# Kernel tuning notes

Measured on AMD Instinct MI355X. Metric: run time of the kernel, lower is better.

The kernel has to match this reference:

```python
import jax, jax.numpy as jnp
import numpy as np

B, NINP, NMAX, C = 32, 16, 128, 128

def conv1x1(x, w, b):
    # x: [B, cin, n, n], w: [cout, cin], b: [cout]
    return jnp.einsum('bchw,oc->bohw', x, w) + b[None, :, None, None]

def block(x, Msum, wa, ba, wb, bb, wc, bc):
    x1 = jax.nn.relu(conv1x1(x, wa, ba) * Msum)
    x2 = jax.nn.relu(conv1x1(x, wb, bb) * Msum)
    x1x2 = jnp.matmul(x1, x2) * Msum          # batched [B,C,n,n] @ [B,C,n,n]
    return jax.nn.relu(conv1x1(jnp.concatenate([x1x2, x], axis=1), wc, bc) * Msum)

def setup_inputs() -> dict:
    key = jax.random.key(0)
    ks = jax.random.split(key, 32)
    def w(k, o, i, s=0.05):
        return jax.random.normal(k, (o, i), dtype=jnp.float32) * s
    inp = {
        'X2': jax.random.normal(ks[0], (B, NINP, NMAX, NMAX), dtype=jnp.float32),
        'M':  jax.random.uniform(ks[1], (B, 2, NMAX, NMAX), dtype=jnp.float32),
        'w11': w(ks[2], C, NINP), 'b11': jnp.zeros((C,), jnp.float32),
        'w12': w(ks[3], C, NINP), 'b12': jnp.zeros((C,), jnp.float32),
        'w13': w(ks[4], C, C + NINP), 'b13': jnp.zeros((C,), jnp.float32),
        'w21': w(ks[5], C, C), 'b21': jnp.zeros((C,), jnp.float32),
        'w22': w(ks[6], C, C), 'b22': jnp.zeros((C,), jnp.float32),
        'w23': w(ks[7], C, 2 * C), 'b23': jnp.zeros((C,), jnp.float32),
        'w31': w(ks[8], C, C), 'b31': jnp.zeros((C,), jnp.float32),
        'w32': w(ks[9], C, C), 'b32': jnp.zeros((C,), jnp.float32),
        'w33': w(ks[10], C, 2 * C), 'b33': jnp.zeros((C,), jnp.float32),
        'h1w': w(ks[11], 32, 3 * C), 'h1b': jnp.zeros((32,), jnp.float32),
        'h2w': w(ks[12], 1, 32), 'h2b': jnp.zeros((1,), jnp.float32),
    }
    return inp

def reference(X2, M, w11, b11, w12, b12, w13, b13, w21, b21, w22, b22, w23, b23,
              w31, b31, w32, b32, w33, b33, h1w, h1b, h2w, h2b):
    Msum = jnp.sum(M, axis=1, keepdims=True)   # [B,1,n,n]
    Mdiag = M[:, 0:1]                          # [B,1,n,n]
    x = X2
    x = block(x, Msum, w11, b11, w12, b12, w13, b13)
    xo1 = jnp.sum(x * Mdiag, axis=(2, 3))      # [B,C]
    x = block(x, Msum, w21, b21, w22, b22, w23, b23)
    xo2 = jnp.sum(x * Mdiag, axis=(2, 3))
    x = block(x, Msum, w31, b31, w32, b32, w33, b33)
    xo3 = jnp.sum(x * Mdiag, axis=(2, 3))
    h = jnp.concatenate([xo1, xo2, xo3], axis=1)
    h = jax.nn.relu(h @ h1w.T + h1b)
    return h @ h2w.T + h2b                     # [B,1]
```

## Files before the change

### kernel.cpp

```cpp
#include <hip/hip_runtime.h>
#include <stdint.h>
#include <stddef.h>

#define NBATCH 32
#define HW     16384
#define CCH    128
#define WROW   40
#define WCHUNK 10240

typedef short bf16x8 __attribute__((ext_vector_type(8)));
typedef float f32x4  __attribute__((ext_vector_type(4)));

__device__ __forceinline__ float bf2f(unsigned short u){
    union { unsigned int i; float f; } v; v.i = ((unsigned int)u) << 16; return v.f;
}
__device__ __forceinline__ unsigned short f2bf(float f){
    union { float f; unsigned int i; } v; v.f = f;
    unsigned int x = v.i;
    x += 0x7fffu + ((x >> 16) & 1u);
    return (unsigned short)(x >> 16);
}
__device__ __forceinline__ unsigned int h16(uint2 u, int j){
    unsigned int v = (j & 2) ? u.y : u.x;
    return (j & 1) ? (v >> 16) : (v & 0xffffu);
}
__device__ __forceinline__ void gl_lds16(const unsigned short* g, unsigned short* l){
    __builtin_amdgcn_global_load_lds(
        reinterpret_cast<const __attribute__((address_space(1))) unsigned int*>(
            reinterpret_cast<uintptr_t>(g)),
        reinterpret_cast<__attribute__((address_space(3))) unsigned int*>(
            reinterpret_cast<uintptr_t>(l)),
        16, 0, 0);
}

#define WPREP_TOTAL 399360
__global__ __launch_bounds__(256) void k_prep(
    const float* __restrict__ w11, const float* __restrict__ w12, const float* __restrict__ w13,
    const float* __restrict__ w21, const float* __restrict__ w22, const float* __restrict__ w23,
    const float* __restrict__ w31, const float* __restrict__ w32, const float* __restrict__ w33,
    unsigned short* __restrict__ wp)
{
    int i = blockIdx.x*256 + threadIdx.x;
    if(i >= WPREP_TOTAL) return;
    const float* src; int K, mode, base;
    if     (i < 10240) { src=w11; K=16;  mode=1; base=0;      }
    else if(i < 20480) { src=w12; K=16;  mode=1; base=10240;  }
    else if(i < 71680) { src=w13; K=144; mode=2; base=20480;  }
    else if(i < 112640){ src=w21; K=128; mode=0; base=71680;  }
    else if(i < 153600){ src=w22; K=128; mode=0; base=112640; }
    else if(i < 235520){ src=w23; K=256; mode=0; base=153600; }
    else if(i < 276480){ src=w31; K=128; mode=0; base=235520; }
    else if(i < 317440){ src=w32; K=128; mode=0; base=276480; }
    else               { src=w33; K=256; mode=0; base=317440; }
    int j  = i - base;
    int ck = j / WCHUNK;
    int jj = j - ck*WCHUNK;
    int half = jj / 5120;
    int rr   = (jj / WROW) & 127;
    int c    = jj % WROW;
    float v = 0.f;
    if(c < 32){
        int col = (mode==1) ? (c & 15)
                : (mode==2) ? (ck < 4 ? ck*32 + c : 128 + (c & 15))
                :             ck*32 + c;
        v = src[rr*K + col];
    }
    unsigned short hi = f2bf(v);
    wp[i] = half ? f2bf(v - bf2f(hi)) : hi;
}

__global__ __launch_bounds__(256) void k_msum(const float* __restrict__ M, float* __restrict__ msum){
    int i = blockIdx.x*256 + threadIdx.x;
    int b = i >> 14, hw = i & (HW-1);
    msum[i] = M[(size_t)b*2*HW + hw] + M[(size_t)b*2*HW + HW + hw];
}

template<int NCHP, int NCHX, bool CC, bool XS>
__global__ __launch_bounds__(256,2) void k_conv(
    const unsigned short* __restrict__ Wp,
    const unsigned short* __restrict__ Psrc,
    const void* __restrict__ Xsrc,
    const float* __restrict__ biasA, const float* __restrict__ biasB,
    const float* __restrict__ msum, const float* __restrict__ Mfull,
    unsigned short* __restrict__ OutA, unsigned short* __restrict__ OutB,
    float* __restrict__ xo, int b0, int xo_off)
{
    constexpr int NCH = NCHP + NCHX;
    __shared__ unsigned short Wl[2*WCHUNK];
    __shared__ unsigned short Xt[256*WROW];
    const int bi = blockIdx.y, bg = b0 + bi;
    const int hw0 = blockIdx.x * 256;
    const int z = CC ? 0 : blockIdx.z;
    const int t = threadIdx.x;
    const int w = t >> 6, l = t & 63;
    const int lr = l & 15, lg = l >> 4;
    const int wm = w & 1, wn = w >> 1;
    const int cg = t & 3, h4 = t >> 2;
    const unsigned short* Wseg  = Wp + (size_t)z*NCH*WCHUNK;
    const unsigned short* pbase = (NCHP > 0) ? (Psrc + (size_t)bi*CCH*HW) : nullptr;
    const float* xfbase = nullptr;
    const unsigned short* xbbase = nullptr;
    if constexpr (XS) xfbase = (const float*)Xsrc + (size_t)bg*16*HW;
    else              xbbase = (const unsigned short*)Xsrc + (size_t)bi*CCH*HW;

    f32x4 acc[4][8];
    #pragma unroll
    for(int mf=0; mf<4; mf++)
        #pragma unroll
        for(int nf=0; nf<8; nf++) acc[mf][nf] = (f32x4){0.f,0.f,0.f,0.f};

    uint2 xr0[8], xr1[8];
    float xf0[16], xf1[16];

    auto wdma = [&](int ck){
        const unsigned short* src = Wseg + (size_t)ck*WCHUNK + (size_t)t*8;
        unsigned short* dstl = &Wl[(ck & 1)*WCHUNK + t*8];
        #pragma unroll
        for(int r=0; r<5; r++)
            gl_lds16(src + (size_t)r*2048, dstl + r*2048);
    };
    auto loadXb = [&](int ck, uint2 (&xr)[8]){
        const unsigned short* s = ((ck < NCHP) ? (pbase + (size_t)ck*32*HW)
                                               : (xbbase + (size_t)(ck-NCHP)*32*HW))
                                  + hw0 + h4*4;
        #pragma unroll
        for(int i=0;i<8;i++) xr[i] = *reinterpret_cast<const uint2*>(s + (size_t)(cg*8+i)*HW);
    };
    auto loadXf = [&](float (&xf)[16]){
        const float* s = xfbase + hw0 + t;
        #pragma unroll
        for(int c=0;c<16;c++) xf[c] = s[(size_t)c*HW];
    };
    auto writeXb = [&](uint2 (&xr)[8]){
        #pragma unroll
        for(int j=0;j<4;j++){
            uint4 pk;
            pk.x = h16(xr[0],j) | (h16(xr[1],j) << 16);
            pk.y = h16(xr[2],j) | (h16(xr[3],j) << 16);
            pk.z = h16(xr[4],j) | (h16(xr[5],j) << 16);
            pk.w = h16(xr[6],j) | (h16(xr[7],j) << 16);
            *reinterpret_cast<uint4*>(&Xt[(h4*4+j)*WROW + cg*8]) = pk;
        }
    };
    auto writeXf = [&](float (&xf)[16]){
        unsigned int hi[16], lo[16];
        #pragma unroll
        for(int c=0;c<16;c++){
            unsigned short h = f2bf(xf[c]);
            hi[c] = h;
            lo[c] = f2bf(xf[c] - bf2f(h));
        }
        uint4 a, b2, c4, d;
        a.x  = hi[0] |(hi[1] <<16); a.y  = hi[2] |(hi[3] <<16); a.z  = hi[4] |(hi[5] <<16); a.w  = hi[6] |(hi[7] <<16);
        b2.x = hi[8] |(hi[9] <<16); b2.y = hi[10]|(hi[11]<<16); b2.z = hi[12]|(hi[13]<<16); b2.w = hi[14]|(hi[15]<<16);
        c4.x = lo[0] |(lo[1] <<16); c4.y = lo[2] |(lo[3] <<16); c4.z = lo[4] |(lo[5] <<16); c4.w = lo[6] |(lo[7] <<16);
        d.x  = lo[8] |(lo[9] <<16); d.y  = lo[10]|(lo[11]<<16); d.z  = lo[12]|(lo[13]<<16); d.w  = lo[14]|(lo[15]<<16);
        unsigned short* base = &Xt[t*WROW];
        *reinterpret_cast<uint4*>(base +  0) = a;
        *reinterpret_cast<uint4*>(base +  8) = b2;
        *reinterpret_cast<uint4*>(base + 16) = c4;
        *reinterpret_cast<uint4*>(base + 24) = d;
    };
    auto do_load = [&](int ck, uint2 (&xr)[8], float (&xf)[16]){
        if(ck < NCHP) loadXb(ck, xr);
        else if constexpr (XS) loadXf(xf);
        else loadXb(ck, xr);
    };
    auto do_write = [&](int ck, uint2 (&xr)[8], float (&xf)[16]){
        if(ck < NCHP) writeXb(xr);
        else if constexpr (XS) writeXf(xf);
        else writeXb(xr);
    };
    auto compute = [&](int ck){
        const unsigned short* Wb = &Wl[(ck & 1)*WCHUNK];
        bf16x8 ah[4], al[4];
        #pragma unroll
        for(int mf=0; mf<4; mf++){
            ah[mf] = *reinterpret_cast<const bf16x8*>(&Wb[(wm*64 + mf*16 + lr)*WROW + lg*8]);
            al[mf] = *reinterpret_cast<const bf16x8*>(&Wb[(128 + wm*64 + mf*16 + lr)*WROW + lg*8]);
        }
        #pragma unroll
        for(int nf=0; nf<8; nf++){
            bf16x8 bfr = *reinterpret_cast<const bf16x8*>(&Xt[(wn*128 + nf*16 + lr)*WROW + lg*8]);
            #pragma unroll
            for(int mf=0; mf<4; mf++){
                acc[mf][nf] = __builtin_amdgcn_mfma_f32_16x16x32_bf16(ah[mf], bfr, acc[mf][nf], 0,0,0);
                acc[mf][nf] = __builtin_amdgcn_mfma_f32_16x16x32_bf16(al[mf], bfr, acc[mf][nf], 0,0,0);
            }
        }
    };

    wdma(0);
    do_load(0, xr0, xf0);

    #pragma unroll
    for(int ck=0; ck<NCH; ck+=2){
        do_write(ck, xr0, xf0);
        asm volatile("s_waitcnt vmcnt(0) lgkmcnt(0)" ::: "memory");
        __builtin_amdgcn_s_barrier();
        if(ck+1 < NCH){ wdma(ck+1); do_load(ck+1, xr1, xf1); }
        compute(ck);
        __builtin_amdgcn_s_barrier();
        if(ck+1 < NCH){
            do_write(ck+1, xr1, xf1);
            asm volatile("s_waitcnt vmcnt(0) lgkmcnt(0)" ::: "memory");
            __builtin_amdgcn_s_barrier();
            if(ck+2 < NCH){ wdma(ck+2); do_load(ck+2, xr0, xf0); }
            compute(ck+1);
            __builtin_amdgcn_s_barrier();
        }
    }

    float msv[8], mdv[8];
    #pragma unroll
    for(int nf=0; nf<8; nf++){
        int hwi = hw0 + wn*128 + nf*16 + lr;
        msv[nf] = msum[(size_t)bg*HW + hwi];
        if constexpr (CC) mdv[nf] = Mfull[(size_t)bg*2*HW + hwi];
    }
    const float* bias = z ? biasB : biasA;
    unsigned short* dst = (z ? OutB : OutA) + (size_t)bi*CCH*HW;
    #pragma unroll
    for(int mf=0; mf<4; mf++){
        float red[4] = {0.f,0.f,0.f,0.f};
        #pragma unroll
        for(int reg=0; reg<4; reg++){
            int row = wm*64 + mf*16 + lg*4 + reg;
            float bv = bias[row];
            #pragma unroll
            for(int nf=0; nf<8; nf++){
                float v2 = (acc[mf][nf][reg] + bv) * msv[nf];
                v2 = v2 > 0.f ? v2 : 0.f;
                dst[(size_t)row*HW + hw0 + wn*128 + nf*16 + lr] = f2bf(v2);
                if constexpr (CC) red[reg] += v2 * mdv[nf];
            }
        }
        if constexpr (CC){
            #pragma unroll
            for(int reg=0; reg<4; reg++){
                float r = red[reg];
                r += __shfl_xor(r, 1);
                r += __shfl_xor(r, 2);
                r += __shfl_xor(r, 4);
                r += __shfl_xor(r, 8);
                if(lr == 0)
                    atomicAdd(&xo[(size_t)bg*384 + xo_off + wm*64 + mf*16 + lg*4 + reg], r);
            }
        }
    }
}

__global__ __launch_bounds__(256) void k_bmm(
    const unsigned short* __restrict__ A, const unsigned short* __restrict__ Bm,
    const float* __restrict__ msum, unsigned short* __restrict__ P, int b0)
{
    __shared__ unsigned short Bs[128*136];
    const int m  = blockIdx.x;
    const int bi = m >> 7;
    const int bg = b0 + bi;
    const unsigned short* Ab = A  + (size_t)m*HW;
    const unsigned short* Bb = Bm + (size_t)m*HW;
    unsigned short*       Pb = P  + (size_t)m*HW;
    const float* ms = msum + (size_t)bg*HW;
    const int t = threadIdx.x;
    const int w  = t >> 6;
    const int l  = t & 63;
    const int lr = l & 15;
    const int lg = l >> 4;

    bf16x8 af[4][2];
    #pragma unroll
    for(int kk=0;kk<4;kk++)
        #pragma unroll
        for(int rt=0;rt<2;rt++)
            af[kk][rt] = *reinterpret_cast<const bf16x8*>(Ab + (size_t)(w*32 + rt*16 + lr)*128 + kk*32 + lg*8);

    #pragma unroll
    for(int it=0; it<8; it++){
        int task = it*256 + t;
        int j  = task & 127;
        int kg = task >> 7;
        unsigned short v[8];
        #pragma unroll
        for(int i=0;i<8;i++) v[i] = Bb[(size_t)(kg*8+i)*128 + j];
        uint4 pk;
        pk.x = (unsigned int)v[0] | ((unsigned int)v[1]<<16);
        pk.y = (unsigned int)v[2] | ((unsigned int)v[3]<<16);
        pk.z = (unsigned int)v[4] | ((unsigned int)v[5]<<16);
        pk.w = (unsigned int)v[6] | ((unsigned int)v[7]<<16);
        *reinterpret_cast<uint4*>(&Bs[j*136 + kg*8]) = pk;
    }
    __syncthreads();

    f32x4 acc[2][8];
    #pragma unroll
    for(int rt=0;rt<2;rt++)
        #pragma unroll
        for(int ct=0;ct<8;ct++) acc[rt][ct] = (f32x4){0.f,0.f,0.f,0.f};

    #pragma unroll
    for(int kk=0;kk<4;kk++){
        #pragma unroll
        for(int ct=0;ct<8;ct++){
            bf16x8 bfr = *reinterpret_cast<const bf16x8*>(&Bs[(ct*16+lr)*136 + kk*32 + lg*8]);
            acc[0][ct] = __builtin_amdgcn_mfma_f32_16x16x32_bf16(af[kk][0], bfr, acc[0][ct], 0,0,0);
            acc[1][ct] = __builtin_amdgcn_mfma_f32_16x16x32_bf16(af[kk][1], bfr, acc[1][ct], 0,0,0);
        }
    }
    #pragma unroll
    for(int rt=0;rt<2;rt++){
        #pragma unroll
        for(int ct=0;ct<8;ct++){
            #pragma unroll
            for(int r=0;r<4;r++){
                int row = w*32 + rt*16 + lg*4 + r;
                int col = ct*16 + lr;
                float v = acc[rt][ct][r] * ms[row*128 + col];
                Pb[(size_t)row*128 + col] = f2bf(v);
            }
        }
    }
}

__global__ __launch_bounds__(1024) void k_head(
    const float* __restrict__ xo, const float* __restrict__ h1w, const float* __restrict__ h1b,
    const float* __restrict__ h2w, const float* __restrict__ h2b, float* __restrict__ out)
{
    __shared__ float hbuf[NBATCH][32];
    const int t = threadIdx.x;
    const int b = t >> 5, j = t & 31;
    float a = h1b[j];
    #pragma unroll 8
    for(int k=0;k<384;k++) a += xo[b*384+k]*h1w[j*384+k];
    a = a > 0.f ? a : 0.f;
    hbuf[b][j] = a;
    __syncthreads();
    if(j == 0){
        float s = h2b[0];
        #pragma unroll
        for(int k=0;k<32;k++) s += hbuf[b][k]*h2w[k];
        out[b] = s;
    }
}

extern "C" void kernel_launch(void* const* d_in, const int* in_sizes, int n_in,
                              void* d_out, int out_size, void* d_ws, size_t ws_size,
                              hipStream_t stream)
{
    (void)in_sizes; (void)n_in; (void)out_size;
    const float* X2  = (const float*)d_in[0];
    const float* M   = (const float*)d_in[1];
    const float* w11 = (const float*)d_in[2];  const float* b11 = (const float*)d_in[3];
    const float* w12 = (const float*)d_in[4];  const float* b12 = (const float*)d_in[5];
    const float* w13 = (const float*)d_in[6];  const float* b13 = (const float*)d_in[7];
    const float* w21 = (const float*)d_in[8];  const float* b21 = (const float*)d_in[9];
    const float* w22 = (const float*)d_in[10]; const float* b22 = (const float*)d_in[11];
    const float* w23 = (const float*)d_in[12]; const float* b23 = (const float*)d_in[13];
    const float* w31 = (const float*)d_in[14]; const float* b31 = (const float*)d_in[15];
    const float* w32 = (const float*)d_in[16]; const float* b32 = (const float*)d_in[17];
    const float* w33 = (const float*)d_in[18]; const float* b33 = (const float*)d_in[19];
    const float* h1w = (const float*)d_in[20]; const float* h1b = (const float*)d_in[21];
    const float* h2w = (const float*)d_in[22]; const float* h2b = (const float*)d_in[23];
    float* out = (float*)d_out;

    char* ws = (char*)d_ws;
    size_t off = 0;
    float* msum = (float*)(ws + off); off += (size_t)NBATCH*HW*4;
    float* xo   = (float*)(ws + off); off += (size_t)NBATCH*384*4;
    unsigned short* wp = (unsigned short*)(ws + off); off += (size_t)WPREP_TOTAL*2;
    off = (off + 255) & ~(size_t)255;

    int bc = 32;
    while (bc > 1 && off + 3ull*(size_t)bc*CCH*HW*2 > ws_size) bc >>= 1;
    size_t bufb = (size_t)bc*CCH*HW*2;
    unsigned short* buf0 = (unsigned short*)(ws + off);
    unsigned short* buf1 = (unsigned short*)(ws + off + bufb);
    unsigned short* buf2 = (unsigned short*)(ws + off + 2*bufb);

    const unsigned short* Wa1 = wp + 0;
    const unsigned short* Wc1 = wp + 20480;
    const unsigned short* Wa2 = wp + 71680;
    const unsigned short* Wc2 = wp + 153600;
    const unsigned short* Wa3 = wp + 235520;
    const unsigned short* Wc3 = wp + 317440;

    k_prep<<<(WPREP_TOTAL+255)/256, 256, 0, stream>>>(w11,w12,w13,w21,w22,w23,w31,w32,w33, wp);
    k_msum<<<(NBATCH*HW)/256, 256, 0, stream>>>(M, msum);
    hipMemsetAsync(xo, 0, (size_t)NBATCH*384*4, stream);

    for(int b0 = 0; b0 < NBATCH; b0 += bc){
        dim3 gab(HW/256, bc, 2);
        dim3 gcc(HW/256, bc);
        dim3 gmat(bc*CCH);
        k_conv<0,1,false,true ><<<gab, 256, 0, stream>>>(Wa1, nullptr, X2, b11, b12, msum, M, buf0, buf1, nullptr, b0, 0);
        k_bmm<<<gmat, 256, 0, stream>>>(buf0, buf1, msum, buf0, b0);
        k_conv<4,1,true ,true ><<<gcc, 256, 0, stream>>>(Wc1, buf0, X2, b13, b13, msum, M, buf1, nullptr, xo, b0, 0);
        k_conv<0,4,false,false><<<gab, 256, 0, stream>>>(Wa2, nullptr, buf1, b21, b22, msum, M, buf2, buf0, nullptr, b0, 0);
        k_bmm<<<gmat, 256, 0, stream>>>(buf2, buf0, msum, buf2, b0);
        k_conv<4,4,true ,false><<<gcc, 256, 0, stream>>>(Wc2, buf2, buf1, b23, b23, msum, M, buf0, nullptr, xo, b0, 128);
        k_conv<0,4,false,false><<<gab, 256, 0, stream>>>(Wa3, nullptr, buf0, b31, b32, msum, M, buf1, buf2, nullptr, b0, 0);
        k_bmm<<<gmat, 256, 0, stream>>>(buf1, buf2, msum, buf1, b0);
        k_conv<4,4,true ,false><<<gcc, 256, 0, stream>>>(Wc3, buf1, buf0, b33, b33, msum, M, buf2, nullptr, xo, b0, 256);
    }
    k_head<<<1, 1024, 0, stream>>>(xo, h1w, h1b, h2w, h2b, out);
}
```

Measured before the change: 1.174 ms.

## Pre-swizzle conv inputs into LDS-ready tiles and retile conv to 512 threads

Conv outputs that feed the next block and the input X2 are now written in a pre-tiled, XOR-swizzled bf16 hi/lo layout. The next conv can DMA them straight into LDS with global_load_lds instead of loading registers and transposing. Weight packing drops row padding in favour of the same XOR swizzle to avoid bank conflicts. The conv kernel moves to 512 threads with a smaller per-wave tile and a finer vmcnt-based pipeline. In exchange it adds an X2 prep kernel, an extra workspace buffer and more complex swizzle indexing, and the last block skips storing its output.

```diff
diff --git a/kernel.cpp b/kernel.cpp
--- a/kernel.cpp
+++ b/kernel.cpp
@@ -5,8 +5,6 @@
 #define NBATCH 32
 #define HW     16384
 #define CCH    128
-#define WROW   40
-#define WCHUNK 10240
 
 typedef short bf16x8 __attribute__((ext_vector_type(8)));
 typedef float f32x4  __attribute__((ext_vector_type(4)));
@@ -32,8 +30,11 @@
             reinterpret_cast<uintptr_t>(l)),
         16, 0, 0);
 }
-
-#define WPREP_TOTAL 399360
+template<int N> __device__ __forceinline__ void vmwait(){
+    asm volatile("s_waitcnt vmcnt(%0)" :: "n"(N) : "memory");
+}
+
+#define WPREP_TOTAL 319488
 __global__ __launch_bounds__(256) void k_prep(
     const float* __restrict__ w11, const float* __restrict__ w12, const float* __restrict__ w13,
     const float* __restrict__ w21, const float* __restrict__ w22, const float* __restrict__ w23,
@@ -43,30 +44,53 @@
     int i = blockIdx.x*256 + threadIdx.x;
     if(i >= WPREP_TOTAL) return;
     const float* src; int K, mode, base;
-    if     (i < 10240) { src=w11; K=16;  mode=1; base=0;      }
-    else if(i < 20480) { src=w12; K=16;  mode=1; base=10240;  }
-    else if(i < 71680) { src=w13; K=144; mode=2; base=20480;  }
-    else if(i < 112640){ src=w21; K=128; mode=0; base=71680;  }
-    else if(i < 153600){ src=w22; K=128; mode=0; base=112640; }
-    else if(i < 235520){ src=w23; K=256; mode=0; base=153600; }
-    else if(i < 276480){ src=w31; K=128; mode=0; base=235520; }
-    else if(i < 317440){ src=w32; K=128; mode=0; base=276480; }
-    else               { src=w33; K=256; mode=0; base=317440; }
+    if     (i < 8192)  { src=w11; K=16;  mode=1; base=0;      }
+    else if(i < 16384) { src=w12; K=16;  mode=1; base=8192;   }
+    else if(i < 57344) { src=w13; K=144; mode=2; base=16384;  }
+    else if(i < 90112) { src=w21; K=128; mode=0; base=57344;  }
+    else if(i < 122880){ src=w22; K=128; mode=0; base=90112;  }
+    else if(i < 188416){ src=w23; K=256; mode=0; base=122880; }
+    else if(i < 221184){ src=w31; K=128; mode=0; base=188416; }
+    else if(i < 253952){ src=w32; K=128; mode=0; base=221184; }
+    else               { src=w33; K=256; mode=0; base=253952; }
     int j  = i - base;
-    int ck = j / WCHUNK;
-    int jj = j - ck*WCHUNK;
-    int half = jj / 5120;
-    int rr   = (jj / WROW) & 127;
-    int c    = jj % WROW;
-    float v = 0.f;
-    if(c < 32){
-        int col = (mode==1) ? (c & 15)
-                : (mode==2) ? (ck < 4 ? ck*32 + c : 128 + (c & 15))
-                :             ck*32 + c;
-        v = src[rr*K + col];
-    }
+    int ck = j >> 13;
+    int jj = j & 8191;
+    int half = jj >> 12;
+    int row  = (jj >> 5) & 127;
+    int cs   = jj & 31;
+    int s    = (row >> 1) & 3;
+    int c    = (((cs >> 3) ^ s) << 3) | (cs & 7);
+    int col  = (mode==1) ? (c & 15)
+             : (mode==2) ? (ck < 4 ? ck*32 + c : 128 + (c & 15))
+             :             ck*32 + c;
+    float v = src[row*K + col];
     unsigned short hi = f2bf(v);
     wp[i] = half ? f2bf(v - bf2f(hi)) : hi;
+}
+
+__global__ __launch_bounds__(256) void k_xprep(const float* __restrict__ X2, unsigned short* __restrict__ X2b){
+    const int ht = blockIdx.x, b = blockIdx.y, t = threadIdx.x;
+    const float* src = X2 + (size_t)b*16*HW + ht*256 + t;
+    unsigned short hv[16], lv[16];
+    #pragma unroll
+    for(int c=0;c<16;c++){
+        float v = src[(size_t)c*HW];
+        hv[c] = f2bf(v);
+        lv[c] = f2bf(v - bf2f(hv[c]));
+    }
+    const int s = (t >> 1) & 3;
+    unsigned short* dst = X2b + ((size_t)b*64 + ht)*8192 + t*32;
+    #pragma unroll
+    for(int g=0; g<4; g++){
+        const unsigned short* q = (g < 2) ? &hv[(g&1)*8] : &lv[(g&1)*8];
+        uint4 pk;
+        pk.x = (unsigned int)q[0] | ((unsigned int)q[1]<<16);
+        pk.y = (unsigned int)q[2] | ((unsigned int)q[3]<<16);
+        pk.z = (unsigned int)q[4] | ((unsigned int)q[5]<<16);
+        pk.w = (unsigned int)q[6] | ((unsigned int)q[7]<<16);
+        *reinterpret_cast<uint4*>(dst + ((g ^ s) << 3)) = pk;
+    }
 }
 
 __global__ __launch_bounds__(256) void k_msum(const float* __restrict__ M, float* __restrict__ msum){
@@ -75,167 +99,155 @@
     msum[i] = M[(size_t)b*2*HW + hw] + M[(size_t)b*2*HW + HW + hw];
 }
 
-template<int NCHP, int NCHX, bool CC, bool XS>
-__global__ __launch_bounds__(256,2) void k_conv(
+template<int NCHP, int NCHX, bool CC, bool GX, bool STORE>
+__global__ __launch_bounds__(512,4) void k_conv(
     const unsigned short* __restrict__ Wp,
     const unsigned short* __restrict__ Psrc,
-    const void* __restrict__ Xsrc,
+    const unsigned short* __restrict__ Xsrc,
     const float* __restrict__ biasA, const float* __restrict__ biasB,
     const float* __restrict__ msum, const float* __restrict__ Mfull,
     unsigned short* __restrict__ OutA, unsigned short* __restrict__ OutB,
     float* __restrict__ xo, int b0, int xo_off)
 {
     constexpr int NCH = NCHP + NCHX;
-    __shared__ unsigned short Wl[2*WCHUNK];
-    __shared__ unsigned short Xt[256*WROW];
-    const int bi = blockIdx.y, bg = b0 + bi;
-    const int hw0 = blockIdx.x * 256;
+    __shared__ unsigned short Wl[16384];
+    __shared__ unsigned short Xl[16384];
+    const int bi = blockIdx.y, bg = b0 + bi, ht = blockIdx.x;
     const int z = CC ? 0 : blockIdx.z;
     const int t = threadIdx.x;
-    const int w = t >> 6, l = t & 63;
-    const int lr = l & 15, lg = l >> 4;
+    const int w = t >> 6, lane = t & 63;
+    const int lr = lane & 15, lg = lane >> 4;
     const int wm = w & 1, wn = w >> 1;
-    const int cg = t & 3, h4 = t >> 2;
-    const unsigned short* Wseg  = Wp + (size_t)z*NCH*WCHUNK;
-    const unsigned short* pbase = (NCHP > 0) ? (Psrc + (size_t)bi*CCH*HW) : nullptr;
-    const float* xfbase = nullptr;
-    const unsigned short* xbbase = nullptr;
-    if constexpr (XS) xfbase = (const float*)Xsrc + (size_t)bg*16*HW;
-    else              xbbase = (const unsigned short*)Xsrc + (size_t)bi*CCH*HW;
-
-    f32x4 acc[4][8];
+    const int cg = t & 7, h4 = t >> 3;
+    const unsigned short* Wseg  = Wp + (size_t)z*NCH*8192;
+    const unsigned short* pbase = Psrc + (size_t)bi*CCH*HW;
+    const unsigned short* xbase = Xsrc + ((size_t)(GX ? bg : bi)*64 + ht)*NCHX*8192;
+
+    f32x4 acc[4][4];
     #pragma unroll
     for(int mf=0; mf<4; mf++)
         #pragma unroll
-        for(int nf=0; nf<8; nf++) acc[mf][nf] = (f32x4){0.f,0.f,0.f,0.f};
-
-    uint2 xr0[8], xr1[8];
-    float xf0[16], xf1[16];
-
-    auto wdma = [&](int ck){
-        const unsigned short* src = Wseg + (size_t)ck*WCHUNK + (size_t)t*8;
-        unsigned short* dstl = &Wl[(ck & 1)*WCHUNK + t*8];
-        #pragma unroll
-        for(int r=0; r<5; r++)
-            gl_lds16(src + (size_t)r*2048, dstl + r*2048);
+        for(int nf=0; nf<4; nf++) acc[mf][nf] = (f32x4){0.f,0.f,0.f,0.f};
+
+    uint2 pr[2][4];
+
+    auto stage = [&](int ck){
+        { const unsigned short* s = Wseg + (size_t)ck*8192 + t*8;
+          unsigned short* d = &Wl[(ck&1)*8192] + t*8;
+          gl_lds16(s, d); gl_lds16(s + 4096, d + 4096); }
+        if(ck < NCHP){
+            const unsigned short* s = pbase + (size_t)(ck*32 + cg*4)*HW + ht*256 + h4*4;
+            #pragma unroll
+            for(int i2=0;i2<4;i2++) pr[ck&1][i2] = *reinterpret_cast<const uint2*>(s + (size_t)i2*HW);
+        } else {
+            const unsigned short* s = xbase + (size_t)(ck - NCHP)*8192 + t*8;
+            unsigned short* d = &Xl[(ck&1)*8192] + t*8;
+            gl_lds16(s, d); gl_lds16(s + 4096, d + 4096);
+        }
     };
-    auto loadXb = [&](int ck, uint2 (&xr)[8]){
-        const unsigned short* s = ((ck < NCHP) ? (pbase + (size_t)ck*32*HW)
-                                               : (xbbase + (size_t)(ck-NCHP)*32*HW))
-                                  + hw0 + h4*4;
-        #pragma unroll
-        for(int i=0;i<8;i++) xr[i] = *reinterpret_cast<const uint2*>(s + (size_t)(cg*8+i)*HW);
+    auto writeP = [&](int ck){
+        #pragma unroll
+        for(int j=0;j<4;j++){
+            int hwin = h4*4 + j;
+            int sx = (hwin >> 1) & 3;
+            int pos = (((cg>>1) ^ sx) << 3) + (cg&1)*4;
+            uint2 v;
+            v.x = h16(pr[ck&1][0],j) | (h16(pr[ck&1][1],j) << 16);
+            v.y = h16(pr[ck&1][2],j) | (h16(pr[ck&1][3],j) << 16);
+            *reinterpret_cast<uint2*>(&Xl[(ck&1)*8192] + hwin*32 + pos) = v;
+        }
     };
-    auto loadXf = [&](float (&xf)[16]){
-        const float* s = xfbase + hw0 + t;
-        #pragma unroll
-        for(int c=0;c<16;c++) xf[c] = s[(size_t)c*HW];
+    auto compute = [&](int buf){
+        const unsigned short* Wb = &Wl[buf*8192];
+        const unsigned short* Xb = &Xl[buf*8192];
+        #pragma unroll
+        for(int hp=0; hp<2; hp++){
+            bf16x8 ah[2], al[2];
+            #pragma unroll
+            for(int m2=0;m2<2;m2++){
+                int row = wm*64 + (hp*2+m2)*16 + lr;
+                int off = row*32 + ((lg ^ ((row>>1)&3)) << 3);
+                ah[m2] = *reinterpret_cast<const bf16x8*>(&Wb[off]);
+                al[m2] = *reinterpret_cast<const bf16x8*>(&Wb[4096 + off]);
+            }
+            #pragma unroll
+            for(int nf=0;nf<4;nf++){
+                int hwin = wn*64 + nf*16 + lr;
+                bf16x8 bfr = *reinterpret_cast<const bf16x8*>(&Xb[hwin*32 + ((lg ^ ((hwin>>1)&3)) << 3)]);
+                #pragma unroll
+                for(int m2=0;m2<2;m2++){
+                    acc[hp*2+m2][nf] = __builtin_amdgcn_mfma_f32_16x16x32_bf16(ah[m2], bfr, acc[hp*2+m2][nf], 0,0,0);
+                    acc[hp*2+m2][nf] = __builtin_amdgcn_mfma_f32_16x16x32_bf16(al[m2], bfr, acc[hp*2+m2][nf], 0,0,0);
+                }
+            }
+        }
     };
-    auto writeXb = [&](uint2 (&xr)[8]){
-        #pragma unroll
-        for(int j=0;j<4;j++){
-            uint4 pk;
-            pk.x = h16(xr[0],j) | (h16(xr[1],j) << 16);
-            pk.y = h16(xr[2],j) | (h16(xr[3],j) << 16);
-            pk.z = h16(xr[4],j) | (h16(xr[5],j) << 16);
-            pk.w = h16(xr[6],j) | (h16(xr[7],j) << 16);
-            *reinterpret_cast<uint4*>(&Xt[(h4*4+j)*WROW + cg*8]) = pk;
-        }
-    };
-    auto writeXf = [&](float (&xf)[16]){
-        unsigned int hi[16], lo[16];
-        #pragma unroll
-        for(int c=0;c<16;c++){
-            unsigned short h = f2bf(xf[c]);
-            hi[c] = h;
-            lo[c] = f2bf(xf[c] - bf2f(h));
-        }
-        uint4 a, b2, c4, d;
-        a.x  = hi[0] |(hi[1] <<16); a.y  = hi[2] |(hi[3] <<16); a.z  = hi[4] |(hi[5] <<16); a.w  = hi[6] |(hi[7] <<16);
-        b2.x = hi[8] |(hi[9] <<16); b2.y = hi[10]|(hi[11]<<16); b2.z = hi[12]|(hi[13]<<16); b2.w = hi[14]|(hi[15]<<16);
-        c4.x = lo[0] |(lo[1] <<16); c4.y = lo[2] |(lo[3] <<16); c4.z = lo[4] |(lo[5] <<16); c4.w = lo[6] |(lo[7] <<16);
-        d.x  = lo[8] |(lo[9] <<16); d.y  = lo[10]|(lo[11]<<16); d.z  = lo[12]|(lo[13]<<16); d.w  = lo[14]|(lo[15]<<16);
-        unsigned short* base = &Xt[t*WROW];
-        *reinterpret_cast<uint4*>(base +  0) = a;
-        *reinterpret_cast<uint4*>(base +  8) = b2;
-        *reinterpret_cast<uint4*>(base + 16) = c4;
-        *reinterpret_cast<uint4*>(base + 24) = d;
-    };
-    auto do_load = [&](int ck, uint2 (&xr)[8], float (&xf)[16]){
-        if(ck < NCHP) loadXb(ck, xr);
-        else if constexpr (XS) loadXf(xf);
-        else loadXb(ck, xr);
-    };
-    auto do_write = [&](int ck, uint2 (&xr)[8], float (&xf)[16]){
-        if(ck < NCHP) writeXb(xr);
-        else if constexpr (XS) writeXf(xf);
-        else writeXb(xr);
-    };
-    auto compute = [&](int ck){
-        const unsigned short* Wb = &Wl[(ck & 1)*WCHUNK];
-        bf16x8 ah[4], al[4];
-        #pragma unroll
-        for(int mf=0; mf<4; mf++){
-            ah[mf] = *reinterpret_cast<const bf16x8*>(&Wb[(wm*64 + mf*16 + lr)*WROW + lg*8]);
-            al[mf] = *reinterpret_cast<const bf16x8*>(&Wb[(128 + wm*64 + mf*16 + lr)*WROW + lg*8]);
-        }
-        #pragma unroll
-        for(int nf=0; nf<8; nf++){
-            bf16x8 bfr = *reinterpret_cast<const bf16x8*>(&Xt[(wn*128 + nf*16 + lr)*WROW + lg*8]);
-            #pragma unroll
-            for(int mf=0; mf<4; mf++){
-                acc[mf][nf] = __builtin_amdgcn_mfma_f32_16x16x32_bf16(ah[mf], bfr, acc[mf][nf], 0,0,0);
-                acc[mf][nf] = __builtin_amdgcn_mfma_f32_16x16x32_bf16(al[mf], bfr, acc[mf][nf], 0,0,0);
-            }
-        }
-    };
-
-    wdma(0);
-    do_load(0, xr0, xf0);
-
-    #pragma unroll
-    for(int ck=0; ck<NCH; ck+=2){
-        do_write(ck, xr0, xf0);
-        asm volatile("s_waitcnt vmcnt(0) lgkmcnt(0)" ::: "memory");
+
+    stage(0);
+    #pragma unroll
+    for(int i=0;i<NCH;i++){
+        if(i+1 < NCH) stage(i+1);
+        if(i+1 < NCH){ if(i+1 < NCHP) vmwait<6>(); else vmwait<4>(); }
+        else vmwait<0>();
+        __builtin_amdgcn_sched_barrier(0);
+        if(i < NCHP) writeP(i);
+        asm volatile("s_waitcnt lgkmcnt(0)" ::: "memory");
         __builtin_amdgcn_s_barrier();
-        if(ck+1 < NCH){ wdma(ck+1); do_load(ck+1, xr1, xf1); }
-        compute(ck);
+        compute(i & 1);
         __builtin_amdgcn_s_barrier();
-        if(ck+1 < NCH){
-            do_write(ck+1, xr1, xf1);
-            asm volatile("s_waitcnt vmcnt(0) lgkmcnt(0)" ::: "memory");
-            __builtin_amdgcn_s_barrier();
-            if(ck+2 < NCH){ wdma(ck+2); do_load(ck+2, xr0, xf0); }
-            compute(ck+1);
-            __builtin_amdgcn_s_barrier();
-        }
-    }
-
-    float msv[8], mdv[8];
-    #pragma unroll
-    for(int nf=0; nf<8; nf++){
-        int hwi = hw0 + wn*128 + nf*16 + lr;
+    }
+
+    float msv[4], mdv[4];
+    #pragma unroll
+    for(int nf=0; nf<4; nf++){
+        int hwi = ht*256 + wn*64 + nf*16 + lr;
         msv[nf] = msum[(size_t)bg*HW + hwi];
         if constexpr (CC) mdv[nf] = Mfull[(size_t)bg*2*HW + hwi];
     }
-    const float* bias = z ? biasB : biasA;
-    unsigned short* dst = (z ? OutB : OutA) + (size_t)bi*CCH*HW;
-    #pragma unroll
-    for(int mf=0; mf<4; mf++){
-        float red[4] = {0.f,0.f,0.f,0.f};
-        #pragma unroll
-        for(int reg=0; reg<4; reg++){
-            int row = wm*64 + mf*16 + lg*4 + reg;
-            float bv = bias[row];
-            #pragma unroll
-            for(int nf=0; nf<8; nf++){
-                float v2 = (acc[mf][nf][reg] + bv) * msv[nf];
-                v2 = v2 > 0.f ? v2 : 0.f;
-                dst[(size_t)row*HW + hw0 + wn*128 + nf*16 + lr] = f2bf(v2);
-                if constexpr (CC) red[reg] += v2 * mdv[nf];
-            }
-        }
-        if constexpr (CC){
+    if constexpr (!CC){
+        const float* bias = z ? biasB : biasA;
+        unsigned short* dst = (z ? OutB : OutA) + (size_t)bi*CCH*HW;
+        #pragma unroll
+        for(int mf=0; mf<4; mf++){
+            #pragma unroll
+            for(int reg=0; reg<4; reg++){
+                int row = wm*64 + mf*16 + lg*4 + reg;
+                float bv = bias[row];
+                #pragma unroll
+                for(int nf=0; nf<4; nf++){
+                    float v2 = (acc[mf][nf][reg] + bv) * msv[nf];
+                    v2 = v2 > 0.f ? v2 : 0.f;
+                    dst[(size_t)row*HW + ht*256 + wn*64 + nf*16 + lr] = f2bf(v2);
+                }
+            }
+        }
+    } else {
+        #pragma unroll
+        for(int mf=0; mf<4; mf++){
+            const int ckO = wm*2 + (mf>>1);
+            const int c0  = (mf&1)*16 + lg*4;
+            float red[4] = {0.f,0.f,0.f,0.f};
+            #pragma unroll
+            for(int nf=0; nf<4; nf++){
+                int hwin = wn*64 + nf*16 + lr;
+                float vv[4];
+                #pragma unroll
+                for(int reg=0; reg<4; reg++){
+                    int row = wm*64 + mf*16 + lg*4 + reg;
+                    float v2 = (acc[mf][nf][reg] + biasA[row]) * msv[nf];
+                    v2 = v2 > 0.f ? v2 : 0.f;
+                    vv[reg] = v2;
+                    red[reg] += v2 * mdv[nf];
+                }
+                if constexpr (STORE){
+                    int sx = (hwin>>1)&3;
+                    int pos = ((((c0>>3) ^ sx) << 3)) + (c0 & 7);
+                    uint2 pk;
+                    pk.x = (unsigned int)f2bf(vv[0]) | ((unsigned int)f2bf(vv[1])<<16);
+                    pk.y = (unsigned int)f2bf(vv[2]) | ((unsigned int)f2bf(vv[3])<<16);
+                    *reinterpret_cast<uint2*>(OutA + (((size_t)bi*64 + ht)*4 + ckO)*8192 + hwin*32 + pos) = pk;
+                }
+            }
             #pragma unroll
             for(int reg=0; reg<4; reg++){
                 float r = red[reg];
@@ -367,40 +379,44 @@
     size_t off = 0;
     float* msum = (float*)(ws + off); off += (size_t)NBATCH*HW*4;
     float* xo   = (float*)(ws + off); off += (size_t)NBATCH*384*4;
-    unsigned short* wp = (unsigned short*)(ws + off); off += (size_t)WPREP_TOTAL*2;
+    unsigned short* wp  = (unsigned short*)(ws + off); off += (size_t)WPREP_TOTAL*2;
     off = (off + 255) & ~(size_t)255;
+    unsigned short* X2b = (unsigned short*)(ws + off); off += (size_t)NBATCH*64*8192*2;
+    off = (off + 255) & ~(size_t)255;
 
     int bc = 32;
-    while (bc > 1 && off + 3ull*(size_t)bc*CCH*HW*2 > ws_size) bc >>= 1;
+    while (bc > 1 && off + 4ull*(size_t)bc*CCH*HW*2 > ws_size) bc >>= 1;
     size_t bufb = (size_t)bc*CCH*HW*2;
-    unsigned short* buf0 = (unsigned short*)(ws + off);
-    unsigned short* buf1 = (unsigned short*)(ws + off + bufb);
-    unsigned short* buf2 = (unsigned short*)(ws + off + 2*bufb);
-
-    const unsigned short* Wa1 = wp + 0;
-    const unsigned short* Wc1 = wp + 20480;
-    const unsigned short* Wa2 = wp + 71680;
-    const unsigned short* Wc2 = wp + 153600;
-    const unsigned short* Wa3 = wp + 235520;
-    const unsigned short* Wc3 = wp + 317440;
+    unsigned short* bufA = (unsigned short*)(ws + off);
+    unsigned short* bufB = (unsigned short*)(ws + off + bufb);
+    unsigned short* Xs1  = (unsigned short*)(ws + off + 2*bufb);
+    unsigned short* Xs2  = (unsigned short*)(ws + off + 3*bufb);
+
+    const unsigned short* Wab1 = wp + 0;
+    const unsigned short* Wc1  = wp + 16384;
+    const unsigned short* Wab2 = wp + 57344;
+    const unsigned short* Wc2  = wp + 122880;
+    const unsigned short* Wab3 = wp + 188416;
+    const unsigned short* Wc3  = wp + 253952;
 
     k_prep<<<(WPREP_TOTAL+255)/256, 256, 0, stream>>>(w11,w12,w13,w21,w22,w23,w31,w32,w33, wp);
+    k_xprep<<<dim3(64, NBATCH), 256, 0, stream>>>(X2, X2b);
     k_msum<<<(NBATCH*HW)/256, 256, 0, stream>>>(M, msum);
     hipMemsetAsync(xo, 0, (size_t)NBATCH*384*4, stream);
 
     for(int b0 = 0; b0 < NBATCH; b0 += bc){
-        dim3 gab(HW/256, bc, 2);
-        dim3 gcc(HW/256, bc);
+        dim3 gab(64, bc, 2);
+        dim3 gcc(64, bc, 1);
         dim3 gmat(bc*CCH);
-        k_conv<0,1,false,true ><<<gab, 256, 0, stream>>>(Wa1, nullptr, X2, b11, b12, msum, M, buf0, buf1, nullptr, b0, 0);
-        k_bmm<<<gmat, 256, 0, stream>>>(buf0, buf1, msum, buf0, b0);
-        k_conv<4,1,true ,true ><<<gcc, 256, 0, stream>>>(Wc1, buf0, X2, b13, b13, msum, M, buf1, nullptr, xo, b0, 0);
-        k_conv<0,4,false,false><<<gab, 256, 0, stream>>>(Wa2, nullptr, buf1, b21, b22, msum, M, buf2, buf0, nullptr, b0, 0);
-        k_bmm<<<gmat, 256, 0, stream>>>(buf2, buf0, msum, buf2, b0);
-        k_conv<4,4,true ,false><<<gcc, 256, 0, stream>>>(Wc2, buf2, buf1, b23, b23, msum, M, buf0, nullptr, xo, b0, 128);
-        k_conv<0,4,false,false><<<gab, 256, 0, stream>>>(Wa3, nullptr, buf0, b31, b32, msum, M, buf1, buf2, nullptr, b0, 0);
-        k_bmm<<<gmat, 256, 0, stream>>>(buf1, buf2, msum, buf1, b0);
-        k_conv<4,4,true ,false><<<gcc, 256, 0, stream>>>(Wc3, buf1, buf0, b33, b33, msum, M, buf2, nullptr, xo, b0, 256);
+        k_conv<0,1,false,true ,true ><<<gab, 512, 0, stream>>>(Wab1, bufA, X2b, b11, b12, msum, M, bufA, bufB, xo, b0, 0);
+        k_bmm<<<gmat, 256, 0, stream>>>(bufA, bufB, msum, bufA, b0);
+        k_conv<4,1,true ,true ,true ><<<gcc, 512, 0, stream>>>(Wc1, bufA, X2b, b13, b13, msum, M, Xs1, nullptr, xo, b0, 0);
+        k_conv<0,4,false,false,true ><<<gab, 512, 0, stream>>>(Wab2, bufA, Xs1, b21, b22, msum, M, bufA, bufB, xo, b0, 0);
+        k_bmm<<<gmat, 256, 0, stream>>>(bufA, bufB, msum, bufA, b0);
+        k_conv<4,4,true ,false,true ><<<gcc, 512, 0, stream>>>(Wc2, bufA, Xs1, b23, b23, msum, M, Xs2, nullptr, xo, b0, 128);
+        k_conv<0,4,false,false,true ><<<gab, 512, 0, stream>>>(Wab3, bufA, Xs2, b31, b32, msum, M, bufA, bufB, xo, b0, 0);
+        k_bmm<<<gmat, 256, 0, stream>>>(bufA, bufB, msum, bufA, b0);
+        k_conv<4,4,true ,false,false><<<gcc, 512, 0, stream>>>(Wc3, bufA, Xs2, b33, b33, msum, M, bufB, nullptr, xo, b0, 256);
     }
     k_head<<<1, 1024, 0, stream>>>(xo, h1w, h1b, h2w, h2b, out);
 }
```

Measured after the change: 1.591 ms. +35.5%, slower.

## Double-buffer conv LDS tiles with partial vmcnt waits and skip final block store

Applied to the files above, without the earlier changes.

The conv kernel now double-buffers the activation tile in LDS and fully unrolls the chunk loop into explicit steps. Each step waits only for the older outstanding global loads through partial vmcnt counts, so there is one barrier per chunk instead of two, and compute runs at raised wave priority. The last block's conv no longer writes its output to global memory, since only the masked reduction into xo is consumed. In exchange, LDS use per block doubles for the X tile, which may limit occupancy, and the hand-counted vmcnt values must match the issued load count exactly.

```diff
diff --git a/kernel.cpp b/kernel.cpp
--- a/kernel.cpp
+++ b/kernel.cpp
@@ -31,6 +31,9 @@
         reinterpret_cast<__attribute__((address_space(3))) unsigned int*>(
             reinterpret_cast<uintptr_t>(l)),
         16, 0, 0);
+}
+template<int N> __device__ __forceinline__ void vmwait(){
+    asm volatile("s_waitcnt vmcnt(%0)" :: "n"(N) : "memory");
 }
 
 #define WPREP_TOTAL 399360
@@ -75,7 +78,7 @@
     msum[i] = M[(size_t)b*2*HW + hw] + M[(size_t)b*2*HW + HW + hw];
 }
 
-template<int NCHP, int NCHX, bool CC, bool XS>
+template<int NCHP, int NCHX, bool CC, bool XS, bool STORE>
 __global__ __launch_bounds__(256,2) void k_conv(
     const unsigned short* __restrict__ Wp,
     const unsigned short* __restrict__ Psrc,
@@ -87,7 +90,7 @@
 {
     constexpr int NCH = NCHP + NCHX;
     __shared__ unsigned short Wl[2*WCHUNK];
-    __shared__ unsigned short Xt[256*WROW];
+    __shared__ unsigned short Xt[2*10240];
     const int bi = blockIdx.y, bg = b0 + bi;
     const int hw0 = blockIdx.x * 256;
     const int z = CC ? 0 : blockIdx.z;
@@ -97,7 +100,7 @@
     const int wm = w & 1, wn = w >> 1;
     const int cg = t & 3, h4 = t >> 2;
     const unsigned short* Wseg  = Wp + (size_t)z*NCH*WCHUNK;
-    const unsigned short* pbase = (NCHP > 0) ? (Psrc + (size_t)bi*CCH*HW) : nullptr;
+    const unsigned short* pbase = Psrc + (size_t)bi*CCH*HW;
     const float* xfbase = nullptr;
     const unsigned short* xbbase = nullptr;
     if constexpr (XS) xfbase = (const float*)Xsrc + (size_t)bg*16*HW;
@@ -113,11 +116,11 @@
     float xf0[16], xf1[16];
 
     auto wdma = [&](int ck){
-        const unsigned short* src = Wseg + (size_t)ck*WCHUNK + (size_t)t*8;
-        unsigned short* dstl = &Wl[(ck & 1)*WCHUNK + t*8];
+        const unsigned short* s = Wseg + (size_t)ck*WCHUNK + (size_t)t*8;
+        unsigned short* d = &Wl[(ck & 1)*WCHUNK + t*8];
         #pragma unroll
         for(int r=0; r<5; r++)
-            gl_lds16(src + (size_t)r*2048, dstl + r*2048);
+            gl_lds16(s + (size_t)r*2048, d + r*2048);
     };
     auto loadXb = [&](int ck, uint2 (&xr)[8]){
         const unsigned short* s = ((ck < NCHP) ? (pbase + (size_t)ck*32*HW)
@@ -131,7 +134,7 @@
         #pragma unroll
         for(int c=0;c<16;c++) xf[c] = s[(size_t)c*HW];
     };
-    auto writeXb = [&](uint2 (&xr)[8]){
+    auto writeXb = [&](int buf, uint2 (&xr)[8]){
         #pragma unroll
         for(int j=0;j<4;j++){
             uint4 pk;
@@ -139,10 +142,10 @@
             pk.y = h16(xr[2],j) | (h16(xr[3],j) << 16);
             pk.z = h16(xr[4],j) | (h16(xr[5],j) << 16);
             pk.w = h16(xr[6],j) | (h16(xr[7],j) << 16);
-            *reinterpret_cast<uint4*>(&Xt[(h4*4+j)*WROW + cg*8]) = pk;
-        }
-    };
-    auto writeXf = [&](float (&xf)[16]){
+            *reinterpret_cast<uint4*>(&Xt[buf*10240 + (h4*4+j)*WROW + cg*8]) = pk;
+        }
+    };
+    auto writeXf = [&](int buf, float (&xf)[16]){
         unsigned int hi[16], lo[16];
         #pragma unroll
         for(int c=0;c<16;c++){
@@ -155,24 +158,15 @@
         b2.x = hi[8] |(hi[9] <<16); b2.y = hi[10]|(hi[11]<<16); b2.z = hi[12]|(hi[13]<<16); b2.w = hi[14]|(hi[15]<<16);
         c4.x = lo[0] |(lo[1] <<16); c4.y = lo[2] |(lo[3] <<16); c4.z = lo[4] |(lo[5] <<16); c4.w = lo[6] |(lo[7] <<16);
         d.x  = lo[8] |(lo[9] <<16); d.y  = lo[10]|(lo[11]<<16); d.z  = lo[12]|(lo[13]<<16); d.w  = lo[14]|(lo[15]<<16);
-        unsigned short* base = &Xt[t*WROW];
+        unsigned short* base = &Xt[buf*10240 + t*WROW];
         *reinterpret_cast<uint4*>(base +  0) = a;
         *reinterpret_cast<uint4*>(base +  8) = b2;
         *reinterpret_cast<uint4*>(base + 16) = c4;
         *reinterpret_cast<uint4*>(base + 24) = d;
     };
-    auto do_load = [&](int ck, uint2 (&xr)[8], float (&xf)[16]){
-        if(ck < NCHP) loadXb(ck, xr);
-        else if constexpr (XS) loadXf(xf);
-        else loadXb(ck, xr);
-    };
-    auto do_write = [&](int ck, uint2 (&xr)[8], float (&xf)[16]){
-        if(ck < NCHP) writeXb(xr);
-        else if constexpr (XS) writeXf(xf);
-        else writeXb(xr);
-    };
-    auto compute = [&](int ck){
-        const unsigned short* Wb = &Wl[(ck & 1)*WCHUNK];
+    auto compute = [&](int buf){
+        const unsigned short* Wb = &Wl[buf*WCHUNK];
+        const unsigned short* Xb = &Xt[buf*10240];
         bf16x8 ah[4], al[4];
         #pragma unroll
         for(int mf=0; mf<4; mf++){
@@ -181,7 +175,7 @@
         }
         #pragma unroll
         for(int nf=0; nf<8; nf++){
-            bf16x8 bfr = *reinterpret_cast<const bf16x8*>(&Xt[(wn*128 + nf*16 + lr)*WROW + lg*8]);
+            bf16x8 bfr = *reinterpret_cast<const bf16x8*>(&Xb[(wn*128 + nf*16 + lr)*WROW + lg*8]);
             #pragma unroll
             for(int mf=0; mf<4; mf++){
                 acc[mf][nf] = __builtin_amdgcn_mfma_f32_16x16x32_bf16(ah[mf], bfr, acc[mf][nf], 0,0,0);
@@ -190,26 +184,43 @@
         }
     };
 
+#define LOADC(CK, S) \
+    if constexpr ((CK) < NCHP || !XS){ \
+        if constexpr ((S)==0) loadXb((CK), xr0); else loadXb((CK), xr1); \
+    } else { \
+        if constexpr ((S)==0) loadXf(xf0); else loadXf(xf1); \
+    }
+
+    LOADC(0, 0)
+    __builtin_amdgcn_sched_barrier(0);
     wdma(0);
-    do_load(0, xr0, xf0);
-
-    #pragma unroll
-    for(int ck=0; ck<NCH; ck+=2){
-        do_write(ck, xr0, xf0);
-        asm volatile("s_waitcnt vmcnt(0) lgkmcnt(0)" ::: "memory");
-        __builtin_amdgcn_s_barrier();
-        if(ck+1 < NCH){ wdma(ck+1); do_load(ck+1, xr1, xf1); }
-        compute(ck);
-        __builtin_amdgcn_s_barrier();
-        if(ck+1 < NCH){
-            do_write(ck+1, xr1, xf1);
-            asm volatile("s_waitcnt vmcnt(0) lgkmcnt(0)" ::: "memory");
-            __builtin_amdgcn_s_barrier();
-            if(ck+2 < NCH){ wdma(ck+2); do_load(ck+2, xr0, xf0); }
-            compute(ck+1);
-            __builtin_amdgcn_s_barrier();
-        }
-    }
+    __builtin_amdgcn_sched_barrier(0);
+    if constexpr (NCH > 1){ LOADC(1, 1) }
+    __builtin_amdgcn_sched_barrier(0);
+
+#define STEP(I) \
+    if constexpr ((I) < NCH){ \
+        vmwait<(((I)+1 < NCH) ? ((((I)+1) < NCHP) ? 8 : (XS ? 16 : 8)) : 0)>(); \
+        __builtin_amdgcn_sched_barrier(0); \
+        if constexpr ((I) < NCHP || !XS){ \
+            if constexpr (((I)&1)==0) writeXb((I)&1, xr0); else writeXb((I)&1, xr1); \
+        } else { \
+            if constexpr (((I)&1)==0) writeXf((I)&1, xf0); else writeXf((I)&1, xf1); \
+        } \
+        asm volatile("s_waitcnt lgkmcnt(0)" ::: "memory"); \
+        __builtin_amdgcn_sched_barrier(0); \
+        __builtin_amdgcn_s_barrier(); \
+        if constexpr ((I)+1 < NCH) wdma((I)+1); \
+        __builtin_amdgcn_sched_barrier(0); \
+        if constexpr ((I)+2 < NCH){ LOADC((I)+2, (I)&1) } \
+        __builtin_amdgcn_sched_barrier(0); \
+        __builtin_amdgcn_s_setprio(1); \
+        compute((I)&1); \
+        __builtin_amdgcn_s_setprio(0); \
+    }
+    STEP(0) STEP(1) STEP(2) STEP(3) STEP(4) STEP(5) STEP(6) STEP(7)
+#undef STEP
+#undef LOADC
 
     float msv[8], mdv[8];
     #pragma unroll
@@ -218,24 +229,41 @@
         msv[nf] = msum[(size_t)bg*HW + hwi];
         if constexpr (CC) mdv[nf] = Mfull[(size_t)bg*2*HW + hwi];
     }
-    const float* bias = z ? biasB : biasA;
-    unsigned short* dst = (z ? OutB : OutA) + (size_t)bi*CCH*HW;
-    #pragma unroll
-    for(int mf=0; mf<4; mf++){
-        float red[4] = {0.f,0.f,0.f,0.f};
-        #pragma unroll
-        for(int reg=0; reg<4; reg++){
-            int row = wm*64 + mf*16 + lg*4 + reg;
-            float bv = bias[row];
+    if constexpr (!CC){
+        const float* bias = z ? biasB : biasA;
+        unsigned short* dst = (z ? OutB : OutA) + (size_t)bi*CCH*HW;
+        #pragma unroll
+        for(int mf=0; mf<4; mf++){
             #pragma unroll
-            for(int nf=0; nf<8; nf++){
-                float v2 = (acc[mf][nf][reg] + bv) * msv[nf];
-                v2 = v2 > 0.f ? v2 : 0.f;
-                dst[(size_t)row*HW + hw0 + wn*128 + nf*16 + lr] = f2bf(v2);
-                if constexpr (CC) red[reg] += v2 * mdv[nf];
+            for(int reg=0; reg<4; reg++){
+                int row = wm*64 + mf*16 + lg*4 + reg;
+                float bv = bias[row];
+                #pragma unroll
+                for(int nf=0; nf<8; nf++){
+                    float v2 = (acc[mf][nf][reg] + bv) * msv[nf];
+                    v2 = v2 > 0.f ? v2 : 0.f;
+                    dst[(size_t)row*HW + hw0 + wn*128 + nf*16 + lr] = f2bf(v2);
+                }
             }
         }
-        if constexpr (CC){
+    } else {
+        unsigned short* dst = OutA + (size_t)bi*CCH*HW;
+        #pragma unroll
+        for(int mf=0; mf<4; mf++){
+            float red[4] = {0.f,0.f,0.f,0.f};
+            #pragma unroll
+            for(int reg=0; reg<4; reg++){
+                int row = wm*64 + mf*16 + lg*4 + reg;
+                float bv = biasA[row];
+                #pragma unroll
+                for(int nf=0; nf<8; nf++){
+                    float v2 = (acc[mf][nf][reg] + bv) * msv[nf];
+                    v2 = v2 > 0.f ? v2 : 0.f;
+                    if constexpr (STORE)
+                        dst[(size_t)row*HW + hw0 + wn*128 + nf*16 + lr] = f2bf(v2);
+                    red[reg] += v2 * mdv[nf];
+                }
+            }
             #pragma unroll
             for(int reg=0; reg<4; reg++){
                 float r = red[reg];
@@ -373,9 +401,9 @@
     int bc = 32;
     while (bc > 1 && off + 3ull*(size_t)bc*CCH*HW*2 > ws_size) bc >>= 1;
     size_t bufb = (size_t)bc*CCH*HW*2;
-    unsigned short* buf0 = (unsigned short*)(ws + off);
-    unsigned short* buf1 = (unsigned short*)(ws + off + bufb);
-    unsigned short* buf2 = (unsigned short*)(ws + off + 2*bufb);
+    unsigned short* B0 = (unsigned short*)(ws + off);
+    unsigned short* B1 = (unsigned short*)(ws + off + bufb);
+    unsigned short* B2 = (unsigned short*)(ws + off + 2*bufb);
 
     const unsigned short* Wa1 = wp + 0;
     const unsigned short* Wc1 = wp + 20480;
@@ -392,15 +420,15 @@
         dim3 gab(HW/256, bc, 2);
         dim3 gcc(HW/256, bc);
         dim3 gmat(bc*CCH);
-        k_conv<0,1,false,true ><<<gab, 256, 0, stream>>>(Wa1, nullptr, X2, b11, b12, msum, M, buf0, buf1, nullptr, b0, 0);
-        k_bmm<<<gmat, 256, 0, stream>>>(buf0, buf1, msum, buf0, b0);
-        k_conv<4,1,true ,true ><<<gcc, 256, 0, stream>>>(Wc1, buf0, X2, b13, b13, msum, M, buf1, nullptr, xo, b0, 0);
-        k_conv<0,4,false,false><<<gab, 256, 0, stream>>>(Wa2, nullptr, buf1, b21, b22, msum, M, buf2, buf0, nullptr, b0, 0);
-        k_bmm<<<gmat, 256, 0, stream>>>(buf2, buf0, msum, buf2, b0);
-        k_conv<4,4,true ,false><<<gcc, 256, 0, stream>>>(Wc2, buf2, buf1, b23, b23, msum, M, buf0, nullptr, xo, b0, 128);
-        k_conv<0,4,false,false><<<gab, 256, 0, stream>>>(Wa3, nullptr, buf0, b31, b32, msum, M, buf1, buf2, nullptr, b0, 0);
-        k_bmm<<<gmat, 256, 0, stream>>>(buf1, buf2, msum, buf1, b0);
-        k_conv<4,4,true ,false><<<gcc, 256, 0, stream>>>(Wc3, buf1, buf0, b33, b33, msum, M, buf2, nullptr, xo, b0, 256);
+        k_conv<0,1,false,true ,true ><<<gab, 256, 0, stream>>>(Wa1, B0, X2, b11, b12, msum, M, B0, B1, nullptr, b0, 0);
+        k_bmm<<<gmat, 256, 0, stream>>>(B0, B1, msum, B0, b0);
+        k_conv<4,1,true ,true ,true ><<<gcc, 256, 0, stream>>>(Wc1, B0, X2, b13, b13, msum, M, B1, nullptr, xo, b0, 0);
+        k_conv<0,4,false,false,true ><<<gab, 256, 0, stream>>>(Wa2, B0, B1, b21, b22, msum, M, B2, B0, nullptr, b0, 0);
+        k_bmm<<<gmat, 256, 0, stream>>>(B2, B0, msum, B2, b0);
+        k_conv<4,4,true ,false,true ><<<gcc, 256, 0, stream>>>(Wc2, B2, B1, b23, b23, msum, M, B0, nullptr, xo, b0, 128);
+        k_conv<0,4,false,false,true ><<<gab, 256, 0, stream>>>(Wa3, B2, B0, b31, b32, msum, M, B1, B2, nullptr, b0, 0);
+        k_bmm<<<gmat, 256, 0, stream>>>(B1, B2, msum, B1, b0);
+        k_conv<4,4,true ,false,false><<<gcc, 256, 0, stream>>>(Wc3, B1, B0, b33, b33, msum, M, B2, nullptr, xo, b0, 256);
     }
     k_head<<<1, 1024, 0, stream>>>(xo, h1w, h1b, h2w, h2b, out);
 }
```

Measured after the change: 1.147 ms. -2.3%, faster.
